# Performance work log

Measured on AMD Instinct MI355X. Metric: run time of the kernel, lower is better.

The kernel has to match this reference:

```python
import jax, jax.numpy as jnp
import numpy as np

B, S, D = 64, 2048, 64

def setup_inputs() -> dict:
    key = jax.random.key(0)
    k1, k2, k3, k4 = jax.random.split(key, 4)
    query = jax.random.normal(k1, (B, S, D), dtype=jnp.float32)
    keyt = jax.random.normal(k2, (B, S, D), dtype=jnp.float32)
    value = jax.random.normal(k3, (B, S, D), dtype=jnp.float32)
    mask = jax.random.randint(k4, (1, S, S), 0, 2, dtype=jnp.int32)
    return {"query": query, "key": keyt, "value": value, "mask": mask}

def reference(query, key, value, mask):
    # scores: [B, S, S]
    scale = jnp.sqrt(jnp.asarray(value.shape[-1], dtype=query.dtype))
    scores = jnp.einsum('bqd,bkd->bqk', query, key) / scale
    scores = jnp.where(mask == 0, jnp.asarray(-1e9, dtype=scores.dtype), scores)
    attention_weights = jax.nn.softmax(scores, axis=-1)
    # dropout p=0.0 -> identity
    context = jnp.einsum('bqk,bkd->bqd', attention_weights, value)
    return (context, attention_weights)
```

## Files before the change

### kernel.cpp

```cpp
#include <hip/hip_runtime.h>

#define NB 64
#define NS 2048
#define ND 64
#define KSTEP 32
#define NIT (NS / KSTEP)

typedef __bf16 bf16x8 __attribute__((ext_vector_type(8)));
typedef float f32x4 __attribute__((ext_vector_type(4)));
typedef unsigned int u32;
typedef u32 u32x2 __attribute__((ext_vector_type(2)));
typedef u32 u32x4 __attribute__((ext_vector_type(4)));
typedef unsigned short u16;
typedef u16 u16x4 __attribute__((ext_vector_type(4)));
typedef u16 u16x8 __attribute__((ext_vector_type(8)));

#define TILE_BARRIER()                                   \
  do {                                                   \
    asm volatile("s_waitcnt lgkmcnt(0)" ::: "memory");   \
    __builtin_amdgcn_s_barrier();                        \
    asm volatile("" ::: "memory");                       \
  } while (0)

__device__ __forceinline__ u16 f2bs(float x) {
  __bf16 h = (__bf16)x;
  return __builtin_bit_cast(u16, h);
}

__device__ __forceinline__ bf16x8 cvt8(f32x4 a, f32x4 b) {
  bf16x8 r;
  r[0] = (__bf16)a[0]; r[1] = (__bf16)a[1]; r[2] = (__bf16)a[2]; r[3] = (__bf16)a[3];
  r[4] = (__bf16)b[0]; r[5] = (__bf16)b[1]; r[6] = (__bf16)b[2]; r[7] = (__bf16)b[3];
  return r;
}

__global__ __launch_bounds__(256) void prep_cast_k(const float* __restrict__ K,
                                                   u16* __restrict__ Kbf) {
  const size_t i = ((size_t)blockIdx.x * 256 + threadIdx.x) * 8;
  f32x4 a = __builtin_nontemporal_load((const f32x4*)(K + i));
  f32x4 b = __builtin_nontemporal_load((const f32x4*)(K + i + 4));
  *(bf16x8*)(Kbf + i) = cvt8(a, b);
}

__global__ __launch_bounds__(256) void prep_transp_v(const float* __restrict__ V,
                                                     u16* __restrict__ VT) {
  __shared__ __attribute__((aligned(16))) u16 T[64][72];
  const int b = blockIdx.x >> 5, kt = blockIdx.x & 31;
  const float* src = V + ((size_t)b * NS + kt * 64) * ND;
  {
    const int k = threadIdx.x >> 2, d0 = (threadIdx.x & 3) * 16;
    const float* p = src + (size_t)k * ND + d0;
    f32x4 a0 = __builtin_nontemporal_load((const f32x4*)p);
    f32x4 a1 = __builtin_nontemporal_load((const f32x4*)(p + 4));
    f32x4 a2 = __builtin_nontemporal_load((const f32x4*)(p + 8));
    f32x4 a3 = __builtin_nontemporal_load((const f32x4*)(p + 12));
    *(bf16x8*)&T[k][d0]     = cvt8(a0, a1);
    *(bf16x8*)&T[k][d0 + 8] = cvt8(a2, a3);
  }
  __syncthreads();
  const int d = threadIdx.x >> 2, k0 = (threadIdx.x & 3) * 16;
  u16x8 r0, r1;
#pragma unroll
  for (int j = 0; j < 8; ++j) { r0[j] = T[k0 + j][d]; r1[j] = T[k0 + 8 + j][d]; }
  u16* dst = VT + ((size_t)b * ND + d) * NS + kt * 64 + k0;
  *(u16x8*)dst = r0;
  *(u16x8*)(dst + 8) = r1;
}

__global__ __launch_bounds__(256) void prep_pack_mask(const int* __restrict__ M,
                                                      unsigned long long* __restrict__ Mb) {
  const size_t i = (size_t)blockIdx.x * 256 + threadIdx.x;
  const unsigned long long bal = __ballot(M[i] != 0);
  if ((threadIdx.x & 63) == 0) Mb[i >> 6] = bal;
}

template <bool PRE>
__global__ __launch_bounds__(512, 4) void DotProductAttention_22436909154804_kernel(
    const float* __restrict__ Q, const float* __restrict__ K,
    const float* __restrict__ V, const int* __restrict__ M,
    const u16* __restrict__ Kbf, const u16* __restrict__ VTbf,
    const u32* __restrict__ Mb, float* __restrict__ ctx, float* __restrict__ wts) {
  __shared__ __attribute__((aligned(16))) u16 Kt[2][32][72];
  __shared__ __attribute__((aligned(16))) u16 Vt[2][64][40];

  const int tid  = threadIdx.x;
  const int lane = tid & 63;
  const int w    = tid >> 6;
  const int g    = lane >> 4;
  const int c    = lane & 15;

  const int bid = blockIdx.x;
  const int vb  = (bid & 7) * 128 + (bid >> 3);
  const int b   = vb >> 4;
  const int qt  = vb & 15;
  const int q0w = qt * 128 + w * 16;
  const size_t bq = (size_t)b * NS;

  const float* qp = Q + (bq + q0w + c) * ND + 8 * g;
  f32x4 qa = __builtin_nontemporal_load((const f32x4*)qp);
  f32x4 qb = __builtin_nontemporal_load((const f32x4*)(qp + 4));
  const bf16x8 qf0 = cvt8(qa, qb);
  qa = __builtin_nontemporal_load((const f32x4*)(qp + 32));
  qb = __builtin_nontemporal_load((const f32x4*)(qp + 36));
  const bf16x8 qf1 = cvt8(qa, qb);

  const u16* Kbb = PRE ? (Kbf + bq * ND) : (const u16*)nullptr;
  const u16* VTb = PRE ? (VTbf + bq * ND) : (const u16*)nullptr;
  const float* Kb32 = K + bq * ND;
  const float* Vb32 = V + bq * ND;
  const int* Mr  = M + (size_t)(q0w + c) * NS;
  const u32* Mbr = Mb + (size_t)(q0w + c) * (NS / 32);

  const bool isK = tid < 256;
  const int st   = tid & 255;

  auto msel = [](float e, u32 mm, int idx) -> float {
    u32 keep = (u32)(((int)(mm << (31 - idx))) >> 31);
    return __uint_as_float(__float_as_uint(e) & keep);
  };

  u16x4 k1p;
  u16x8 s2p;
  f32x4 kf0, kf1;
  auto issueK1 = [&](int kb) {
    if (PRE) {
      const int r = tid >> 4, cc = (tid & 15) * 4;
      k1p = *(const u16x4*)(Kbb + (size_t)(kb + r) * ND + cc);
    } else if (isK) {
      const int r = st >> 3, cc = (st & 7) * 8;
      const float* p = Kb32 + (size_t)(kb + r) * ND + cc;
      kf0 = *(const f32x4*)p; kf1 = *(const f32x4*)(p + 4);
    }
  };
  auto writeK1 = [&](int buf) {
    if (PRE) {
      const int r = tid >> 4, cc = (tid & 15) * 4;
      *(u16x4*)&Kt[buf][r][cc] = k1p;
    } else if (isK) {
      const int r = st >> 3, cc = (st & 7) * 8;
      *(bf16x8*)&Kt[buf][r][cc] = cvt8(kf0, kf1);
    }
  };
  auto issueKV = [&](int kb) {
    if (PRE) {
      if (isK) {
        const int r = st >> 3, cc = (st & 7) * 8;
        s2p = *(const u16x8*)(Kbb + (size_t)(kb + r) * ND + cc);
      } else {
        const int d = st >> 2, kc = (st & 3) * 8;
        s2p = *(const u16x8*)(VTb + (size_t)d * NS + kb + kc);
      }
    } else {
      if (isK) {
        const int r = st >> 3, cc = (st & 7) * 8;
        const float* p = Kb32 + (size_t)(kb + r) * ND + cc;
        kf0 = *(const f32x4*)p; kf1 = *(const f32x4*)(p + 4);
      } else {
        const int svp = st >> 4, svd = (st & 15) * 4;
        const float* p = Vb32 + (size_t)(kb + 2 * svp) * ND + svd;
        kf0 = *(const f32x4*)p; kf1 = *(const f32x4*)(p + ND);
      }
    }
  };
  auto writeKV = [&](int buf) {
    if (PRE) {
      if (isK) {
        const int r = st >> 3, cc = (st & 7) * 8;
        *(u16x8*)&Kt[buf][r][cc] = s2p;
      } else {
        const int d = st >> 2, kc = (st & 3) * 8;
        *(u16x8*)&Vt[buf][d][kc] = s2p;
      }
    } else {
      if (isK) {
        const int r = st >> 3, cc = (st & 7) * 8;
        *(bf16x8*)&Kt[buf][r][cc] = cvt8(kf0, kf1);
      } else {
        const int svp = st >> 4, svd = (st & 15) * 4;
#pragma unroll
        for (int j = 0; j < 4; ++j)
          *(u32*)&Vt[buf][svd + j][2 * svp] = (u32)f2bs(kf0[j]) | ((u32)f2bs(kf1[j]) << 16);
      }
    }
  };

  const f32x4 zz = {0.f, 0.f, 0.f, 0.f};

  float rs = 0.f;
  issueK1(0);
  writeK1(0);
  __syncthreads();
  for (int it = 0; it < NIT; ++it) {
    const int cur = it & 1, kb = it * KSTEP;
    if (it + 1 < NIT) issueK1(kb + KSTEP);
    u32 mm = 0;
    if (PRE) mm = Mbr[kb >> 5];
#pragma unroll
    for (int j = 0; j < 2; ++j) {
      bf16x8 a0 = *(const bf16x8*)&Kt[cur][16 * j + c][8 * g];
      bf16x8 a1 = *(const bf16x8*)&Kt[cur][16 * j + c][32 + 8 * g];
      f32x4 s = __builtin_amdgcn_mfma_f32_16x16x32_bf16(a0, qf0, zz, 0, 0, 0);
      s = __builtin_amdgcn_mfma_f32_16x16x32_bf16(a1, qf1, s, 0, 0, 0);
      if (PRE) {
        rs += msel(__expf(s[0] * 0.125f), mm, 16 * j + 4 * g + 0)
            + msel(__expf(s[1] * 0.125f), mm, 16 * j + 4 * g + 1)
            + msel(__expf(s[2] * 0.125f), mm, 16 * j + 4 * g + 2)
            + msel(__expf(s[3] * 0.125f), mm, 16 * j + 4 * g + 3);
      } else {
        const int4 m4 = *(const int4*)(Mr + kb + 16 * j + 4 * g);
        rs += (m4.x ? __expf(s[0] * 0.125f) : 0.f)
            + (m4.y ? __expf(s[1] * 0.125f) : 0.f)
            + (m4.z ? __expf(s[2] * 0.125f) : 0.f)
            + (m4.w ? __expf(s[3] * 0.125f) : 0.f);
      }
    }
    if (it + 1 < NIT) writeK1((it + 1) & 1);
    TILE_BARRIER();
  }
  rs += __shfl_xor(rs, 16);
  rs += __shfl_xor(rs, 32);
  const float lninv = -__logf(rs);

  f32x4 acc[4] = {zz, zz, zz, zz};
  issueKV(0);
  writeKV(0);
  __syncthreads();
  float* wrow = wts + (bq + q0w + c) * NS;
  for (int it = 0; it < NIT; ++it) {
    const int cur = it & 1, kb = it * KSTEP;
    if (it + 1 < NIT) issueKV(kb + KSTEP);
    u32 mm = 0;
    if (PRE) mm = Mbr[kb >> 5];

    u32 wpk[4];
#pragma unroll
    for (int j = 0; j < 2; ++j) {
      bf16x8 a0 = *(const bf16x8*)&Kt[cur][16 * j + c][8 * g];
      bf16x8 a1 = *(const bf16x8*)&Kt[cur][16 * j + c][32 + 8 * g];
      f32x4 s = __builtin_amdgcn_mfma_f32_16x16x32_bf16(a0, qf0, zz, 0, 0, 0);
      s = __builtin_amdgcn_mfma_f32_16x16x32_bf16(a1, qf1, s, 0, 0, 0);
      float w0, w1, w2, w3;
      if (PRE) {
        w0 = msel(__expf(fmaf(s[0], 0.125f, lninv)), mm, 16 * j + 4 * g + 0);
        w1 = msel(__expf(fmaf(s[1], 0.125f, lninv)), mm, 16 * j + 4 * g + 1);
        w2 = msel(__expf(fmaf(s[2], 0.125f, lninv)), mm, 16 * j + 4 * g + 2);
        w3 = msel(__expf(fmaf(s[3], 0.125f, lninv)), mm, 16 * j + 4 * g + 3);
      } else {
        const int4 m4 = *(const int4*)(Mr + kb + 16 * j + 4 * g);
        w0 = m4.x ? __expf(fmaf(s[0], 0.125f, lninv)) : 0.f;
        w1 = m4.y ? __expf(fmaf(s[1], 0.125f, lninv)) : 0.f;
        w2 = m4.z ? __expf(fmaf(s[2], 0.125f, lninv)) : 0.f;
        w3 = m4.w ? __expf(fmaf(s[3], 0.125f, lninv)) : 0.f;
      }
      f32x4 wv = {w0, w1, w2, w3};
      __builtin_nontemporal_store(wv, (f32x4*)(wrow + kb + 16 * j + 4 * g));
      wpk[2 * j]     = (u32)f2bs(w0) | ((u32)f2bs(w1) << 16);
      wpk[2 * j + 1] = (u32)f2bs(w2) | ((u32)f2bs(w3) << 16);
    }

    u32x4 wu = {wpk[0], wpk[1], wpk[2], wpk[3]};
    bf16x8 wb = __builtin_bit_cast(bf16x8, wu);
#pragma unroll
    for (int dt = 0; dt < 4; ++dt) {
      u32x2 vlo = *(const u32x2*)&Vt[cur][dt * 16 + c][4 * g];
      u32x2 vhi = *(const u32x2*)&Vt[cur][dt * 16 + c][16 + 4 * g];
      u32x4 vau = {vlo.x, vlo.y, vhi.x, vhi.y};
      acc[dt] = __builtin_amdgcn_mfma_f32_16x16x32_bf16(
          __builtin_bit_cast(bf16x8, vau), wb, acc[dt], 0, 0, 0);
    }

    if (it + 1 < NIT) writeKV((it + 1) & 1);
    TILE_BARRIER();
  }

  float* crow = ctx + (bq + q0w + c) * ND;
#pragma unroll
  for (int dt = 0; dt < 4; ++dt)
    __builtin_nontemporal_store(acc[dt], (f32x4*)(crow + dt * 16 + 4 * g));
}

extern "C" void kernel_launch(void* const* d_in, const int* in_sizes, int n_in,
                              void* d_out, int out_size, void* d_ws, size_t ws_size,
                              hipStream_t stream) {
  const float* Q = (const float*)d_in[0];
  const float* K = (const float*)d_in[1];
  const float* V = (const float*)d_in[2];
  const int*   M = (const int*)d_in[3];
  float* ctx = (float*)d_out;
  float* wts = (float*)d_out + (size_t)NB * NS * ND;

  dim3 grid(NB * (NS / 128));
  dim3 block(512);

  constexpr size_t KBF_B = (size_t)NB * NS * ND * 2;
  constexpr size_t MB_B  = (size_t)NS * NS / 8;
  u16* Kbf = (u16*)d_ws;
  u16* VTb = (u16*)((char*)d_ws + KBF_B);
  unsigned long long* Mb64 = (unsigned long long*)((char*)d_ws + 2 * KBF_B);

  if (ws_size >= 2 * KBF_B + MB_B) {
    hipLaunchKernelGGL(prep_cast_k, dim3(NB * NS * ND / 8 / 256), dim3(256), 0, stream, K, Kbf);
    hipLaunchKernelGGL(prep_transp_v, dim3(NB * (NS / 64)), dim3(256), 0, stream, V, VTb);
    hipLaunchKernelGGL(prep_pack_mask, dim3(NS * NS / 256), dim3(256), 0, stream, M, Mb64);
    hipLaunchKernelGGL(DotProductAttention_22436909154804_kernel<true>, grid, block, 0, stream,
                       Q, K, V, M, Kbf, VTb, (const u32*)Mb64, ctx, wts);
  } else {
    hipLaunchKernelGGL(DotProductAttention_22436909154804_kernel<false>, grid, block, 0, stream,
                       Q, K, V, M, (const u16*)nullptr, (const u16*)nullptr,
                       (const u32*)nullptr, ctx, wts);
  }
}
```

Measured before the change: 395.8 us.

## Split key dimension across warp pairs with 64-query blocks and exp2 softmax

Each block now handles 64 queries instead of 128, and its 8 warps form two groups that each take half of a 64-key step. Partial row sums and context accumulators are combined through shared memory at the end. The V transpose prep kernel permutes key order so the PRE path can read V fragments with a single 16-byte LDS load, and exp/log are replaced with exp2/log2 using a folded scale. The aim is more parallelism per query tile and fewer LDS instructions. The cost is doubled K/V shared-memory staging per query, extra reduction syncs and lower occupancy bounds.

```diff
diff --git a/kernel.cpp b/kernel.cpp
--- a/kernel.cpp
+++ b/kernel.cpp
@@ -3,7 +3,7 @@
 #define NB 64
 #define NS 2048
 #define ND 64
-#define KSTEP 32
+#define KSTEP 64
 #define NIT (NS / KSTEP)
 
 typedef __bf16 bf16x8 __attribute__((ext_vector_type(8)));
@@ -12,8 +12,24 @@
 typedef u32 u32x2 __attribute__((ext_vector_type(2)));
 typedef u32 u32x4 __attribute__((ext_vector_type(4)));
 typedef unsigned short u16;
-typedef u16 u16x4 __attribute__((ext_vector_type(4)));
 typedef u16 u16x8 __attribute__((ext_vector_type(8)));
+
+#define C2F 0.18033688011112042f
+
+__device__ __forceinline__ float fexp2(float x) {
+#if __has_builtin(__builtin_amdgcn_exp2f)
+  return __builtin_amdgcn_exp2f(x);
+#else
+  return exp2f(x);
+#endif
+}
+__device__ __forceinline__ float flog2(float x) {
+#if __has_builtin(__builtin_amdgcn_logf)
+  return __builtin_amdgcn_logf(x);
+#else
+  return log2f(x);
+#endif
+}
 
 #define TILE_BARRIER()                                   \
   do {                                                   \
@@ -61,7 +77,13 @@
   const int d = threadIdx.x >> 2, k0 = (threadIdx.x & 3) * 16;
   u16x8 r0, r1;
 #pragma unroll
-  for (int j = 0; j < 8; ++j) { r0[j] = T[k0 + j][d]; r1[j] = T[k0 + 8 + j][d]; }
+  for (int j = 0; j < 8; ++j) {
+    const int P0 = k0 + j, P1 = k0 + 8 + j;
+    const int s0 = 32 * (P0 >> 5) + 16 * ((P0 >> 2) & 1) + 4 * ((P0 >> 3) & 3) + (P0 & 3);
+    const int s1 = 32 * (P1 >> 5) + 16 * ((P1 >> 2) & 1) + 4 * ((P1 >> 3) & 3) + (P1 & 3);
+    r0[j] = T[s0][d];
+    r1[j] = T[s1][d];
+  }
   u16* dst = VT + ((size_t)b * ND + d) * NS + kt * 64 + k0;
   *(u16x8*)dst = r0;
   *(u16x8*)(dst + 8) = r1;
@@ -75,25 +97,28 @@
 }
 
 template <bool PRE>
-__global__ __launch_bounds__(512, 4) void DotProductAttention_22436909154804_kernel(
+__global__ __launch_bounds__(512, 3) void DotProductAttention_22436909154804_kernel(
     const float* __restrict__ Q, const float* __restrict__ K,
     const float* __restrict__ V, const int* __restrict__ M,
     const u16* __restrict__ Kbf, const u16* __restrict__ VTbf,
     const u32* __restrict__ Mb, float* __restrict__ ctx, float* __restrict__ wts) {
-  __shared__ __attribute__((aligned(16))) u16 Kt[2][32][72];
-  __shared__ __attribute__((aligned(16))) u16 Vt[2][64][40];
+  __shared__ __attribute__((aligned(16))) u16 Kt[2][64][72];
+  __shared__ __attribute__((aligned(16))) u16 Vt[2][64][72];
+  __shared__ float Rs[2][64];
 
   const int tid  = threadIdx.x;
   const int lane = tid & 63;
   const int w    = tid >> 6;
+  const int wq   = w & 3;
+  const int kt   = w >> 2;
   const int g    = lane >> 4;
   const int c    = lane & 15;
 
   const int bid = blockIdx.x;
-  const int vb  = (bid & 7) * 128 + (bid >> 3);
-  const int b   = vb >> 4;
-  const int qt  = vb & 15;
-  const int q0w = qt * 128 + w * 16;
+  const int vb  = (bid & 7) * 256 + (bid >> 3);
+  const int b   = vb >> 5;
+  const int qt  = vb & 31;
+  const int q0w = qt * 64 + wq * 16;
   const size_t bq = (size_t)b * NS;
 
   const float* qp = Q + (bq + q0w + c) * ND + 8 * g;
@@ -108,8 +133,8 @@
   const u16* VTb = PRE ? (VTbf + bq * ND) : (const u16*)nullptr;
   const float* Kb32 = K + bq * ND;
   const float* Vb32 = V + bq * ND;
-  const int* Mr  = M + (size_t)(q0w + c) * NS;
-  const u32* Mbr = Mb + (size_t)(q0w + c) * (NS / 32);
+  const int* Mr  = M + (size_t)(q0w + c) * NS + kt * 32;
+  const u32* Mbr = Mb + (size_t)(q0w + c) * (NS / 32) + kt;
 
   const bool isK = tid < 256;
   const int st   = tid & 255;
@@ -119,67 +144,76 @@
     return __uint_as_float(__float_as_uint(e) & keep);
   };
 
-  u16x4 k1p;
-  u16x8 s2p;
-  f32x4 kf0, kf1;
+  u16x8 sp0, sp1;
+  f32x4 kf0, kf1, kf2, kf3;
   auto issueK1 = [&](int kb) {
     if (PRE) {
-      const int r = tid >> 4, cc = (tid & 15) * 4;
-      k1p = *(const u16x4*)(Kbb + (size_t)(kb + r) * ND + cc);
+      const int r = tid >> 3, cc = (tid & 7) * 8;
+      sp0 = *(const u16x8*)(Kbb + (size_t)(kb + r) * ND + cc);
     } else if (isK) {
-      const int r = st >> 3, cc = (st & 7) * 8;
+      const int r = st >> 2, cc = (st & 3) * 16;
       const float* p = Kb32 + (size_t)(kb + r) * ND + cc;
-      kf0 = *(const f32x4*)p; kf1 = *(const f32x4*)(p + 4);
+      kf0 = *(const f32x4*)p;       kf1 = *(const f32x4*)(p + 4);
+      kf2 = *(const f32x4*)(p + 8); kf3 = *(const f32x4*)(p + 12);
     }
   };
   auto writeK1 = [&](int buf) {
     if (PRE) {
-      const int r = tid >> 4, cc = (tid & 15) * 4;
-      *(u16x4*)&Kt[buf][r][cc] = k1p;
+      const int r = tid >> 3, cc = (tid & 7) * 8;
+      *(u16x8*)&Kt[buf][r][cc] = sp0;
     } else if (isK) {
-      const int r = st >> 3, cc = (st & 7) * 8;
-      *(bf16x8*)&Kt[buf][r][cc] = cvt8(kf0, kf1);
+      const int r = st >> 2, cc = (st & 3) * 16;
+      *(bf16x8*)&Kt[buf][r][cc]     = cvt8(kf0, kf1);
+      *(bf16x8*)&Kt[buf][r][cc + 8] = cvt8(kf2, kf3);
     }
   };
   auto issueKV = [&](int kb) {
     if (PRE) {
       if (isK) {
-        const int r = st >> 3, cc = (st & 7) * 8;
-        s2p = *(const u16x8*)(Kbb + (size_t)(kb + r) * ND + cc);
-      } else {
-        const int d = st >> 2, kc = (st & 3) * 8;
-        s2p = *(const u16x8*)(VTb + (size_t)d * NS + kb + kc);
+        const int r = st >> 2, cc = (st & 3) * 16;
+        const u16* p = Kbb + (size_t)(kb + r) * ND + cc;
+        sp0 = *(const u16x8*)p; sp1 = *(const u16x8*)(p + 8);
+      } else {
+        const int d = st >> 2, kc = (st & 3) * 16;
+        const u16* p = VTb + (size_t)d * NS + kb + kc;
+        sp0 = *(const u16x8*)p; sp1 = *(const u16x8*)(p + 8);
       }
     } else {
       if (isK) {
-        const int r = st >> 3, cc = (st & 7) * 8;
+        const int r = st >> 2, cc = (st & 3) * 16;
         const float* p = Kb32 + (size_t)(kb + r) * ND + cc;
-        kf0 = *(const f32x4*)p; kf1 = *(const f32x4*)(p + 4);
-      } else {
-        const int svp = st >> 4, svd = (st & 15) * 4;
-        const float* p = Vb32 + (size_t)(kb + 2 * svp) * ND + svd;
-        kf0 = *(const f32x4*)p; kf1 = *(const f32x4*)(p + ND);
+        kf0 = *(const f32x4*)p;       kf1 = *(const f32x4*)(p + 4);
+        kf2 = *(const f32x4*)(p + 8); kf3 = *(const f32x4*)(p + 12);
+      } else {
+        const int k = st >> 2, d0 = (st & 3) * 16;
+        const float* p = Vb32 + (size_t)(kb + k) * ND + d0;
+        kf0 = *(const f32x4*)p;       kf1 = *(const f32x4*)(p + 4);
+        kf2 = *(const f32x4*)(p + 8); kf3 = *(const f32x4*)(p + 12);
       }
     }
   };
   auto writeKV = [&](int buf) {
     if (PRE) {
       if (isK) {
-        const int r = st >> 3, cc = (st & 7) * 8;
-        *(u16x8*)&Kt[buf][r][cc] = s2p;
-      } else {
-        const int d = st >> 2, kc = (st & 3) * 8;
-        *(u16x8*)&Vt[buf][d][kc] = s2p;
+        const int r = st >> 2, cc = (st & 3) * 16;
+        *(u16x8*)&Kt[buf][r][cc] = sp0; *(u16x8*)&Kt[buf][r][cc + 8] = sp1;
+      } else {
+        const int d = st >> 2, kc = (st & 3) * 16;
+        *(u16x8*)&Vt[buf][d][kc] = sp0; *(u16x8*)&Vt[buf][d][kc + 8] = sp1;
       }
     } else {
       if (isK) {
-        const int r = st >> 3, cc = (st & 7) * 8;
-        *(bf16x8*)&Kt[buf][r][cc] = cvt8(kf0, kf1);
-      } else {
-        const int svp = st >> 4, svd = (st & 15) * 4;
-#pragma unroll
-        for (int j = 0; j < 4; ++j)
-          *(u32*)&Vt[buf][svd + j][2 * svp] = (u32)f2bs(kf0[j]) | ((u32)f2bs(kf1[j]) << 16);
+        const int r = st >> 2, cc = (st & 3) * 16;
+        *(bf16x8*)&Kt[buf][r][cc]     = cvt8(kf0, kf1);
+        *(bf16x8*)&Kt[buf][r][cc + 8] = cvt8(kf2, kf3);
+      } else {
+        const int k = st >> 2, d0 = (st & 3) * 16;
+        bf16x8 v0 = cvt8(kf0, kf1), v1 = cvt8(kf2, kf3);
+#pragma unroll
+        for (int j = 0; j < 8; ++j) {
+          Vt[buf][d0 + j][k]     = __builtin_bit_cast(u16, v0[j]);
+          Vt[buf][d0 + 8 + j][k] = __builtin_bit_cast(u16, v1[j]);
+        }
       }
     }
   };
@@ -197,21 +231,21 @@
     if (PRE) mm = Mbr[kb >> 5];
 #pragma unroll
     for (int j = 0; j < 2; ++j) {
-      bf16x8 a0 = *(const bf16x8*)&Kt[cur][16 * j + c][8 * g];
-      bf16x8 a1 = *(const bf16x8*)&Kt[cur][16 * j + c][32 + 8 * g];
+      bf16x8 a0 = *(const bf16x8*)&Kt[cur][kt * 32 + 16 * j + c][8 * g];
+      bf16x8 a1 = *(const bf16x8*)&Kt[cur][kt * 32 + 16 * j + c][32 + 8 * g];
       f32x4 s = __builtin_amdgcn_mfma_f32_16x16x32_bf16(a0, qf0, zz, 0, 0, 0);
       s = __builtin_amdgcn_mfma_f32_16x16x32_bf16(a1, qf1, s, 0, 0, 0);
       if (PRE) {
-        rs += msel(__expf(s[0] * 0.125f), mm, 16 * j + 4 * g + 0)
-            + msel(__expf(s[1] * 0.125f), mm, 16 * j + 4 * g + 1)
-            + msel(__expf(s[2] * 0.125f), mm, 16 * j + 4 * g + 2)
-            + msel(__expf(s[3] * 0.125f), mm, 16 * j + 4 * g + 3);
+        rs += msel(fexp2(s[0] * C2F), mm, 16 * j + 4 * g + 0)
+            + msel(fexp2(s[1] * C2F), mm, 16 * j + 4 * g + 1)
+            + msel(fexp2(s[2] * C2F), mm, 16 * j + 4 * g + 2)
+            + msel(fexp2(s[3] * C2F), mm, 16 * j + 4 * g + 3);
       } else {
         const int4 m4 = *(const int4*)(Mr + kb + 16 * j + 4 * g);
-        rs += (m4.x ? __expf(s[0] * 0.125f) : 0.f)
-            + (m4.y ? __expf(s[1] * 0.125f) : 0.f)
-            + (m4.z ? __expf(s[2] * 0.125f) : 0.f)
-            + (m4.w ? __expf(s[3] * 0.125f) : 0.f);
+        rs += (m4.x ? fexp2(s[0] * C2F) : 0.f)
+            + (m4.y ? fexp2(s[1] * C2F) : 0.f)
+            + (m4.z ? fexp2(s[2] * C2F) : 0.f)
+            + (m4.w ? fexp2(s[3] * C2F) : 0.f);
       }
     }
     if (it + 1 < NIT) writeK1((it + 1) & 1);
@@ -219,13 +253,15 @@
   }
   rs += __shfl_xor(rs, 16);
   rs += __shfl_xor(rs, 32);
-  const float lninv = -__logf(rs);
+  issueKV(0);
+  if (lane < 16) Rs[kt][wq * 16 + c] = rs;
+  __syncthreads();
+  const float l2inv = -flog2(Rs[0][wq * 16 + c] + Rs[1][wq * 16 + c]);
+  writeKV(0);
+  __syncthreads();
 
   f32x4 acc[4] = {zz, zz, zz, zz};
-  issueKV(0);
-  writeKV(0);
-  __syncthreads();
-  float* wrow = wts + (bq + q0w + c) * NS;
+  float* wrow = wts + (bq + q0w + c) * NS + kt * 32;
   for (int it = 0; it < NIT; ++it) {
     const int cur = it & 1, kb = it * KSTEP;
     if (it + 1 < NIT) issueKV(kb + KSTEP);
@@ -235,22 +271,22 @@
     u32 wpk[4];
 #pragma unroll
     for (int j = 0; j < 2; ++j) {
-      bf16x8 a0 = *(const bf16x8*)&Kt[cur][16 * j + c][8 * g];
-      bf16x8 a1 = *(const bf16x8*)&Kt[cur][16 * j + c][32 + 8 * g];
+      bf16x8 a0 = *(const bf16x8*)&Kt[cur][kt * 32 + 16 * j + c][8 * g];
+      bf16x8 a1 = *(const bf16x8*)&Kt[cur][kt * 32 + 16 * j + c][32 + 8 * g];
       f32x4 s = __builtin_amdgcn_mfma_f32_16x16x32_bf16(a0, qf0, zz, 0, 0, 0);
       s = __builtin_amdgcn_mfma_f32_16x16x32_bf16(a1, qf1, s, 0, 0, 0);
       float w0, w1, w2, w3;
       if (PRE) {
-        w0 = msel(__expf(fmaf(s[0], 0.125f, lninv)), mm, 16 * j + 4 * g + 0);
-        w1 = msel(__expf(fmaf(s[1], 0.125f, lninv)), mm, 16 * j + 4 * g + 1);
-        w2 = msel(__expf(fmaf(s[2], 0.125f, lninv)), mm, 16 * j + 4 * g + 2);
-        w3 = msel(__expf(fmaf(s[3], 0.125f, lninv)), mm, 16 * j + 4 * g + 3);
+        w0 = msel(fexp2(fmaf(s[0], C2F, l2inv)), mm, 16 * j + 4 * g + 0);
+        w1 = msel(fexp2(fmaf(s[1], C2F, l2inv)), mm, 16 * j + 4 * g + 1);
+        w2 = msel(fexp2(fmaf(s[2], C2F, l2inv)), mm, 16 * j + 4 * g + 2);
+        w3 = msel(fexp2(fmaf(s[3], C2F, l2inv)), mm, 16 * j + 4 * g + 3);
       } else {
         const int4 m4 = *(const int4*)(Mr + kb + 16 * j + 4 * g);
-        w0 = m4.x ? __expf(fmaf(s[0], 0.125f, lninv)) : 0.f;
-        w1 = m4.y ? __expf(fmaf(s[1], 0.125f, lninv)) : 0.f;
-        w2 = m4.z ? __expf(fmaf(s[2], 0.125f, lninv)) : 0.f;
-        w3 = m4.w ? __expf(fmaf(s[3], 0.125f, lninv)) : 0.f;
+        w0 = m4.x ? fexp2(fmaf(s[0], C2F, l2inv)) : 0.f;
+        w1 = m4.y ? fexp2(fmaf(s[1], C2F, l2inv)) : 0.f;
+        w2 = m4.z ? fexp2(fmaf(s[2], C2F, l2inv)) : 0.f;
+        w3 = m4.w ? fexp2(fmaf(s[3], C2F, l2inv)) : 0.f;
       }
       f32x4 wv = {w0, w1, w2, w3};
       __builtin_nontemporal_store(wv, (f32x4*)(wrow + kb + 16 * j + 4 * g));
@@ -262,21 +298,37 @@
     bf16x8 wb = __builtin_bit_cast(bf16x8, wu);
 #pragma unroll
     for (int dt = 0; dt < 4; ++dt) {
-      u32x2 vlo = *(const u32x2*)&Vt[cur][dt * 16 + c][4 * g];
-      u32x2 vhi = *(const u32x2*)&Vt[cur][dt * 16 + c][16 + 4 * g];
-      u32x4 vau = {vlo.x, vlo.y, vhi.x, vhi.y};
-      acc[dt] = __builtin_amdgcn_mfma_f32_16x16x32_bf16(
-          __builtin_bit_cast(bf16x8, vau), wb, acc[dt], 0, 0, 0);
+      bf16x8 va;
+      if (PRE) {
+        va = *(const bf16x8*)&Vt[cur][dt * 16 + c][kt * 32 + 8 * g];
+      } else {
+        u32x2 vlo = *(const u32x2*)&Vt[cur][dt * 16 + c][kt * 32 + 4 * g];
+        u32x2 vhi = *(const u32x2*)&Vt[cur][dt * 16 + c][kt * 32 + 16 + 4 * g];
+        u32x4 vau = {vlo.x, vlo.y, vhi.x, vhi.y};
+        va = __builtin_bit_cast(bf16x8, vau);
+      }
+      acc[dt] = __builtin_amdgcn_mfma_f32_16x16x32_bf16(va, wb, acc[dt], 0, 0, 0);
     }
 
     if (it + 1 < NIT) writeKV((it + 1) & 1);
     TILE_BARRIER();
   }
 
-  float* crow = ctx + (bq + q0w + c) * ND;
-#pragma unroll
-  for (int dt = 0; dt < 4; ++dt)
-    __builtin_nontemporal_store(acc[dt], (f32x4*)(crow + dt * 16 + 4 * g));
+  float* red = (float*)&Kt[0][0][0] + wq * 1088;
+  if (kt == 1) {
+#pragma unroll
+    for (int dt = 0; dt < 4; ++dt)
+      *(f32x4*)&red[c * 68 + dt * 16 + 4 * g] = acc[dt];
+  }
+  __syncthreads();
+  if (kt == 0) {
+    float* crow = ctx + (bq + q0w + c) * ND;
+#pragma unroll
+    for (int dt = 0; dt < 4; ++dt) {
+      f32x4 vv = acc[dt] + *(const f32x4*)&red[c * 68 + dt * 16 + 4 * g];
+      __builtin_nontemporal_store(vv, (f32x4*)(crow + dt * 16 + 4 * g));
+    }
+  }
 }
 
 extern "C" void kernel_launch(void* const* d_in, const int* in_sizes, int n_in,
@@ -289,7 +341,7 @@
   float* ctx = (float*)d_out;
   float* wts = (float*)d_out + (size_t)NB * NS * ND;
 
-  dim3 grid(NB * (NS / 128));
+  dim3 grid(NB * (NS / 64));
   dim3 block(512);
 
   constexpr size_t KBF_B = (size_t)NB * NS * ND * 2;
```

New measurement: 346.0 us. 12.6% less time.
